# Kernel tuning notes

Measured on AMD Instinct MI355X. Metric: run time of the kernel, lower is better.

Reference implementation:

```python
import jax, jax.numpy as jnp
import numpy as np

B, T, V, D, H = 128, 512, 32000, 300, 128


def setup_inputs() -> dict:
    key = jax.random.key(0)
    ks = jax.random.split(key, 10)
    s = 0.05
    return {
        "encoder_input": jax.random.randint(ks[0], (B, T), 0, V, dtype=jnp.int32),
        "state_fwd": jax.random.normal(ks[1], (B, H), jnp.float32) * s,
        "state_back": jax.random.normal(ks[2], (B, H), jnp.float32) * s,
        "emb": jax.random.normal(ks[3], (V, D), jnp.float32) * s,
        "W_f": jax.random.normal(ks[4], (D, 3 * H), jnp.float32) * s,
        "U_f": jax.random.normal(ks[5], (H, 3 * H), jnp.float32) * s,
        "b_f": jax.random.normal(ks[6], (2, 3 * H), jnp.float32) * s,
        "W_b": jax.random.normal(ks[7], (D, 3 * H), jnp.float32) * s,
        "U_b": jax.random.normal(ks[8], (H, 3 * H), jnp.float32) * s,
        "b_b": jax.random.normal(ks[9], (2, 3 * H), jnp.float32) * s,
    }


def _gru(x, h0, W, U, b):
    # Keras GRU, reset_after=True, eval mode (dropout off).
    b_i, b_r = b[0], b[1]
    xp = jnp.einsum('btd,dg->btg', x, W) + b_i      # precompute input projections [B,T,3H]
    xp = jnp.swapaxes(xp, 0, 1)                     # time-major [T,B,3H]

    def step(h, xpt):
        rec = h @ U + b_r                           # [B,3H]
        xz, xr, xh = jnp.split(xpt, 3, axis=-1)
        rz, rr, rh = jnp.split(rec, 3, axis=-1)
        z = jax.nn.sigmoid(xz + rz)
        r = jax.nn.sigmoid(xr + rr)
        hh = jnp.tanh(xh + r * rh)
        hn = z * h + (1.0 - z) * hh
        return hn, hn

    hT, ys = jax.lax.scan(step, h0, xp)
    return jnp.swapaxes(ys, 0, 1), hT               # [B,T,H], [B,H]


def reference(encoder_input, state_fwd, state_back, emb, W_f, U_f, b_f, W_b, U_b, b_b):
    x = emb[encoder_input]                          # [B,T,D] embedding lookup
    out_f, h_f = _gru(x, state_fwd, W_f, U_f, b_f)
    out_b_rev, h_b = _gru(x[:, ::-1], state_back, W_b, U_b, b_b)
    out_b = out_b_rev[:, ::-1]
    encoder_output = jnp.concatenate([out_f, out_b], axis=-1)  # [B,T,2H]
    return encoder_output, h_f, h_b
```

## Files before the change

### kernel.cpp

```cpp
#include <hip/hip_runtime.h>
#include <stddef.h>

#define BB   128
#define TT   512
#define VV   32000
#define DD   300
#define HH   128
#define G3   384
#define NC   768

typedef __fp16 half_t;
typedef __fp16 half2_t __attribute__((ext_vector_type(2)));
typedef _Float16 f16x8 __attribute__((ext_vector_type(8)));
typedef float    f32x4 __attribute__((ext_vector_type(4)));

union FragF {
    f16x8    v;
    _Float16 h[8];
    f32x4    f4;
};

#define ASTR 40
__global__ __launch_bounds__(256) void proj_kernel(
    const float* __restrict__ emb,
    const float* __restrict__ Wf, const float* __restrict__ Wb,
    const float* __restrict__ bf, const float* __restrict__ bb,
    float* __restrict__ P)
{
    __shared__ __align__(16) _Float16 As[128][ASTR];
    __shared__ __align__(16) _Float16 Bs[128][ASTR];

    const int m0 = blockIdx.x * 128;
    const int n0 = blockIdx.y * 128;

    const float* Wsrc;
    const float* bsrc;
    int cb;
    if (n0 < G3) { Wsrc = Wf; bsrc = bf; cb = n0; }
    else         { Wsrc = Wb; bsrc = bb; cb = n0 - G3; }

    const int t  = threadIdx.x;
    const int w  = t >> 6;
    const int l  = t & 63;
    const int lr = l & 15;
    const int lg = l >> 4;

    f32x4 acc[2][8];
    #pragma unroll
    for (int i = 0; i < 2; ++i)
        #pragma unroll
        for (int j = 0; j < 8; ++j)
            acc[i][j] = (f32x4){0.f, 0.f, 0.f, 0.f};

    const int sm = t & 127;
    const int sh = t >> 7;

    for (int kt = 0; kt < 10; ++kt) {
        const int kb = kt * 32 + sh * 16;

        {
            float v[16];
            if (kt < 9) {
                const float4* src = (const float4*)(emb + (size_t)(m0 + sm) * DD + kb);
                float4 v0 = src[0], v1 = src[1], v2 = src[2], v3 = src[3];
                v[0]=v0.x; v[1]=v0.y; v[2]=v0.z; v[3]=v0.w;
                v[4]=v1.x; v[5]=v1.y; v[6]=v1.z; v[7]=v1.w;
                v[8]=v2.x; v[9]=v2.y; v[10]=v2.z; v[11]=v2.w;
                v[12]=v3.x; v[13]=v3.y; v[14]=v3.z; v[15]=v3.w;
            } else {
                #pragma unroll
                for (int j = 0; j < 16; ++j) {
                    int k = kb + j;
                    v[j] = (k < DD) ? emb[(size_t)(m0 + sm) * DD + k] : 0.f;
                }
            }
            half2_t p[8];
            #pragma unroll
            for (int j = 0; j < 8; ++j)
                p[j] = __builtin_amdgcn_cvt_pkrtz(v[2*j], v[2*j+1]);
            *(float4*)&As[sm][sh * 16]     = *(float4*)&p[0];
            *(float4*)&As[sm][sh * 16 + 8] = *(float4*)&p[4];
        }
        {
            float v[16];
            #pragma unroll
            for (int j = 0; j < 16; ++j) {
                int k = kb + j;
                v[j] = (k < DD) ? Wsrc[(size_t)k * G3 + cb + sm] : 0.f;
            }
            half2_t p[8];
            #pragma unroll
            for (int j = 0; j < 8; ++j)
                p[j] = __builtin_amdgcn_cvt_pkrtz(v[2*j], v[2*j+1]);
            *(float4*)&Bs[sm][sh * 16]     = *(float4*)&p[0];
            *(float4*)&Bs[sm][sh * 16 + 8] = *(float4*)&p[4];
        }
        __syncthreads();

        FragF a[2], bfr[8];
        #pragma unroll
        for (int mf = 0; mf < 2; ++mf)
            a[mf].f4 = *(const f32x4*)&As[lr + 16 * (2 * w + mf)][lg * 8];
        #pragma unroll
        for (int nf = 0; nf < 8; ++nf)
            bfr[nf].f4 = *(const f32x4*)&Bs[lr + 16 * nf][lg * 8];
        #pragma unroll
        for (int mf = 0; mf < 2; ++mf)
            #pragma unroll
            for (int nf = 0; nf < 8; ++nf)
                acc[mf][nf] = __builtin_amdgcn_mfma_f32_16x16x32_f16(
                    a[mf].v, bfr[nf].v, acc[mf][nf], 0, 0, 0);
        __syncthreads();
    }

    float bias_v[8];
    #pragma unroll
    for (int nf = 0; nf < 8; ++nf) bias_v[nf] = bsrc[cb + 16 * nf + lr];

    #pragma unroll
    for (int mf = 0; mf < 2; ++mf)
        #pragma unroll
        for (int nf = 0; nf < 8; ++nf)
            #pragma unroll
            for (int r = 0; r < 4; ++r) {
                int row = m0 + 16 * (2 * w + mf) + lg * 4 + r;
                int col = n0 + 16 * nf + lr;
                P[(size_t)row * NC + col] = acc[mf][nf][r] + bias_v[nf];
            }
}

template<int CTRL>
__device__ __forceinline__ float qp_add(float x) {
    union { float f; int i; } a, r;
    a.f = x;
    r.i = __builtin_amdgcn_update_dpp(0, a.i, CTRL, 0xF, 0xF, true);
    return x + r.f;
}

#define BAR() asm volatile("s_waitcnt lgkmcnt(0)\n\ts_barrier" ::: "memory")

__global__ __launch_bounds__(512)
__attribute__((amdgpu_waves_per_eu(2, 2)))
void scan_kernel(
    const int*   __restrict__ tokens,
    const float* __restrict__ state_f, const float* __restrict__ state_b,
    const float* __restrict__ Uf, const float* __restrict__ Ub,
    const float* __restrict__ bf, const float* __restrict__ bb,
    const float* __restrict__ P,
    float* __restrict__ out)
{
    const int b = blockIdx.x;
    const int d = blockIdx.y;
    const int t = threadIdx.x;
    const int s = t & 3;
    const int q = t >> 2;

    const float* U  = d ? Ub : Uf;
    const float* bv = d ? bb : bf;
    const float* st = d ? state_b : state_f;
    const int    cb = d ? G3 : 0;

    __shared__ __align__(16) half_t hs[2][HH];
    __shared__ int tok_s[TT];

    tok_s[t] = tokens[b * TT + t];

    half2_t uz2[16], ur2[16], uh2[16];
    #pragma unroll
    for (int k2 = 0; k2 < 16; ++k2) {
        const float* U0 = U + (size_t)(s * 32 + 2 * k2) * G3;
        const float* U1 = U0 + G3;
        uz2[k2] = __builtin_amdgcn_cvt_pkrtz(U0[q],          U1[q]);
        ur2[k2] = __builtin_amdgcn_cvt_pkrtz(U0[HH + q],     U1[HH + q]);
        uh2[k2] = __builtin_amdgcn_cvt_pkrtz(U0[2 * HH + q], U1[2 * HH + q]);
    }
    const float bz = bv[G3 + q];
    const float br = bv[G3 + HH + q];
    const float bh = bv[G3 + 2 * HH + q];

    float hreg = st[b * HH + q];
    if (t < HH) hs[0][t] = (half_t)st[b * HH + t];
    __syncthreads();

    float xz_n, xr_n, xh_n;
    {
        int tok = tok_s[d ? (TT - 1) : 0];
        const float* pr = P + (size_t)tok * NC + cb;
        xz_n = pr[q]; xr_n = pr[HH + q]; xh_n = pr[2 * HH + q];
    }

    int cur = 0;
    for (int i = 0; i < TT; ++i) {
        const int tcur = d ? (TT - 1 - i) : i;
        const float xz = xz_n, xr = xr_n, xh = xh_n;
        {
            int in1 = (i + 1 < TT) ? (i + 1) : i;
            int tok = tok_s[d ? (TT - 1 - in1) : in1];
            const float* pr = P + (size_t)tok * NC + cb;
            xz_n = pr[q]; xr_n = pr[HH + q]; xh_n = pr[2 * HH + q];
        }

        half2_t hv[16];
        {
            const float4* hp = (const float4*)&hs[cur][s * 32];
            *(float4*)&hv[0]  = hp[0];
            *(float4*)&hv[4]  = hp[1];
            *(float4*)&hv[8]  = hp[2];
            *(float4*)&hv[12] = hp[3];
        }
        float az = 0.f, ar = 0.f, ah = 0.f;
        #pragma unroll
        for (int k2 = 0; k2 < 16; ++k2) {
            az = __builtin_amdgcn_fdot2(hv[k2], uz2[k2], az, false);
            ar = __builtin_amdgcn_fdot2(hv[k2], ur2[k2], ar, false);
            ah = __builtin_amdgcn_fdot2(hv[k2], uh2[k2], ah, false);
        }
        az = qp_add<0xB1>(az); az = qp_add<0x4E>(az);
        ar = qp_add<0xB1>(ar); ar = qp_add<0x4E>(ar);
        ah = qp_add<0xB1>(ah); ah = qp_add<0x4E>(ah);

        float z = __builtin_amdgcn_rcpf(1.f + __expf(-(az + bz + xz)));
        float r = __builtin_amdgcn_rcpf(1.f + __expf(-(ar + br + xr)));
        float ph = xh + r * (ah + bh);
        ph = fminf(fmaxf(ph, -15.f), 15.f);
        float e  = __expf(-2.f * ph);
        float hh = (1.f - e) * __builtin_amdgcn_rcpf(1.f + e);
        float hn = z * hreg + (1.f - z) * hh;
        hreg = hn;

        const int nxt = cur ^ 1;
        if (s == 0) {
            hs[nxt][q] = (half_t)hn;
            out[((size_t)b * TT + tcur) * 256 + d * HH + q] = hn;
        }
        BAR();
        cur = nxt;
    }

    if (s == 0) {
        out[(size_t)BB * TT * 256 + (size_t)d * BB * HH + b * HH + q] = hreg;
    }
}

extern "C" void kernel_launch(void* const* d_in, const int* in_sizes, int n_in,
                              void* d_out, int out_size, void* d_ws, size_t ws_size,
                              hipStream_t stream)
{
    const int*   tokens  = (const int*)  d_in[0];
    const float* state_f = (const float*)d_in[1];
    const float* state_b = (const float*)d_in[2];
    const float* emb     = (const float*)d_in[3];
    const float* W_f     = (const float*)d_in[4];
    const float* U_f     = (const float*)d_in[5];
    const float* b_f     = (const float*)d_in[6];
    const float* W_b     = (const float*)d_in[7];
    const float* U_b     = (const float*)d_in[8];
    const float* b_b     = (const float*)d_in[9];
    float*       out     = (float*)d_out;

    float* P = (float*)d_ws;

    dim3 gp(VV / 128, NC / 128);
    proj_kernel<<<gp, 256, 0, stream>>>(emb, W_f, W_b, b_f, b_b, P);

    dim3 gs(BB, 2);
    scan_kernel<<<gs, 512, 0, stream>>>(tokens, state_f, state_b,
                                        U_f, U_b, b_f, b_b, P, out);
}
```

Before: 427.6 us.

## Use MFMA for recurrent matvec in scan and double-buffer projection tiles

The scan kernel's recurrent h·U product moves from per-thread fdot2 chains plus DPP quad reductions to 16x16x32 f16 MFMA instructions. U fragments stay in registers, each wave owns 16 output columns, and the h row is broadcast across the A operand, so most MFMA rows are redundant work. The next token index is now fetched two steps ahead, and the waves_per_eu hint is dropped. The projection kernel prefetches the next K tile into registers while MFMAs run on the current shared tile, at the cost of an extra barrier per iteration.

```diff
diff --git a/kernel.cpp b/kernel.cpp
--- a/kernel.cpp
+++ b/kernel.cpp
@@ -9,7 +9,6 @@
 #define G3   384
 #define NC   768
 
-typedef __fp16 half_t;
 typedef __fp16 half2_t __attribute__((ext_vector_type(2)));
 typedef _Float16 f16x8 __attribute__((ext_vector_type(8)));
 typedef float    f32x4 __attribute__((ext_vector_type(4)));
@@ -19,6 +18,8 @@
     _Float16 h[8];
     f32x4    f4;
 };
+
+#define BAR() asm volatile("s_waitcnt lgkmcnt(0)\n\ts_barrier" ::: "memory")
 
 #define ASTR 40
 __global__ __launch_bounds__(256) void proj_kernel(
@@ -55,47 +56,51 @@
     const int sm = t & 127;
     const int sh = t >> 7;
 
+    float va[16], vb[16];
+
+#define LOAD_TILE(KT)                                                         \
+    {                                                                         \
+        const int kb_ = (KT) * 32 + sh * 16;                                  \
+        if ((KT) < 9) {                                                       \
+            const float4* srcA = (const float4*)(emb + (size_t)(m0 + sm) * DD + kb_); \
+            float4 a0 = srcA[0], a1 = srcA[1], a2 = srcA[2], a3 = srcA[3];    \
+            va[0]=a0.x; va[1]=a0.y; va[2]=a0.z; va[3]=a0.w;                   \
+            va[4]=a1.x; va[5]=a1.y; va[6]=a1.z; va[7]=a1.w;                   \
+            va[8]=a2.x; va[9]=a2.y; va[10]=a2.z; va[11]=a2.w;                 \
+            va[12]=a3.x; va[13]=a3.y; va[14]=a3.z; va[15]=a3.w;               \
+            _Pragma("unroll")                                                 \
+            for (int j = 0; j < 16; ++j)                                      \
+                vb[j] = Wsrc[(size_t)(kb_ + j) * G3 + cb + sm];               \
+        } else {                                                              \
+            _Pragma("unroll")                                                 \
+            for (int j = 0; j < 16; ++j) {                                    \
+                int k_ = kb_ + j;                                             \
+                va[j] = (k_ < DD) ? emb[(size_t)(m0 + sm) * DD + k_] : 0.f;   \
+                vb[j] = (k_ < DD) ? Wsrc[(size_t)k_ * G3 + cb + sm] : 0.f;    \
+            }                                                                 \
+        }                                                                     \
+    }
+
+#define STORE_TILE()                                                          \
+    {                                                                         \
+        half2_t pa[8], pb[8];                                                 \
+        _Pragma("unroll")                                                     \
+        for (int j = 0; j < 8; ++j) {                                         \
+            pa[j] = __builtin_amdgcn_cvt_pkrtz(va[2*j], va[2*j+1]);           \
+            pb[j] = __builtin_amdgcn_cvt_pkrtz(vb[2*j], vb[2*j+1]);           \
+        }                                                                     \
+        *(float4*)&As[sm][sh * 16]     = *(float4*)&pa[0];                    \
+        *(float4*)&As[sm][sh * 16 + 8] = *(float4*)&pa[4];                    \
+        *(float4*)&Bs[sm][sh * 16]     = *(float4*)&pb[0];                    \
+        *(float4*)&Bs[sm][sh * 16 + 8] = *(float4*)&pb[4];                    \
+    }
+
+    LOAD_TILE(0);
+    STORE_TILE();
+    BAR();
+
     for (int kt = 0; kt < 10; ++kt) {
-        const int kb = kt * 32 + sh * 16;
-
-        {
-            float v[16];
-            if (kt < 9) {
-                const float4* src = (const float4*)(emb + (size_t)(m0 + sm) * DD + kb);
-                float4 v0 = src[0], v1 = src[1], v2 = src[2], v3 = src[3];
-                v[0]=v0.x; v[1]=v0.y; v[2]=v0.z; v[3]=v0.w;
-                v[4]=v1.x; v[5]=v1.y; v[6]=v1.z; v[7]=v1.w;
-                v[8]=v2.x; v[9]=v2.y; v[10]=v2.z; v[11]=v2.w;
-                v[12]=v3.x; v[13]=v3.y; v[14]=v3.z; v[15]=v3.w;
-            } else {
-                #pragma unroll
-                for (int j = 0; j < 16; ++j) {
-                    int k = kb + j;
-                    v[j] = (k < DD) ? emb[(size_t)(m0 + sm) * DD + k] : 0.f;
-                }
-            }
-            half2_t p[8];
-            #pragma unroll
-            for (int j = 0; j < 8; ++j)
-                p[j] = __builtin_amdgcn_cvt_pkrtz(v[2*j], v[2*j+1]);
-            *(float4*)&As[sm][sh * 16]     = *(float4*)&p[0];
-            *(float4*)&As[sm][sh * 16 + 8] = *(float4*)&p[4];
-        }
-        {
-            float v[16];
-            #pragma unroll
-            for (int j = 0; j < 16; ++j) {
-                int k = kb + j;
-                v[j] = (k < DD) ? Wsrc[(size_t)k * G3 + cb + sm] : 0.f;
-            }
-            half2_t p[8];
-            #pragma unroll
-            for (int j = 0; j < 8; ++j)
-                p[j] = __builtin_amdgcn_cvt_pkrtz(v[2*j], v[2*j+1]);
-            *(float4*)&Bs[sm][sh * 16]     = *(float4*)&p[0];
-            *(float4*)&Bs[sm][sh * 16 + 8] = *(float4*)&p[4];
-        }
-        __syncthreads();
+        if (kt < 9) LOAD_TILE(kt + 1);
 
         FragF a[2], bfr[8];
         #pragma unroll
@@ -110,7 +115,9 @@
             for (int nf = 0; nf < 8; ++nf)
                 acc[mf][nf] = __builtin_amdgcn_mfma_f32_16x16x32_f16(
                     a[mf].v, bfr[nf].v, acc[mf][nf], 0, 0, 0);
-        __syncthreads();
+        BAR();
+        if (kt < 9) STORE_TILE();
+        BAR();
     }
 
     float bias_v[8];
@@ -127,21 +134,11 @@
                 int col = n0 + 16 * nf + lr;
                 P[(size_t)row * NC + col] = acc[mf][nf][r] + bias_v[nf];
             }
+#undef LOAD_TILE
+#undef STORE_TILE
 }
 
-template<int CTRL>
-__device__ __forceinline__ float qp_add(float x) {
-    union { float f; int i; } a, r;
-    a.f = x;
-    r.i = __builtin_amdgcn_update_dpp(0, a.i, CTRL, 0xF, 0xF, true);
-    return x + r.f;
-}
-
-#define BAR() asm volatile("s_waitcnt lgkmcnt(0)\n\ts_barrier" ::: "memory")
-
-__global__ __launch_bounds__(512)
-__attribute__((amdgpu_waves_per_eu(2, 2)))
-void scan_kernel(
+__global__ __launch_bounds__(512) void scan_kernel(
     const int*   __restrict__ tokens,
     const float* __restrict__ state_f, const float* __restrict__ state_b,
     const float* __restrict__ Uf, const float* __restrict__ Ub,
@@ -149,96 +146,96 @@
     const float* __restrict__ P,
     float* __restrict__ out)
 {
-    const int b = blockIdx.x;
-    const int d = blockIdx.y;
-    const int t = threadIdx.x;
-    const int s = t & 3;
-    const int q = t >> 2;
+    const int b  = blockIdx.x;
+    const int d  = blockIdx.y;
+    const int t  = threadIdx.x;
+    const int w  = t >> 6;
+    const int l  = t & 63;
+    const int lr = l & 15;
+    const int lg = l >> 4;
+    const int c  = w * 16 + lr;
 
     const float* U  = d ? Ub : Uf;
     const float* bv = d ? bb : bf;
     const float* st = d ? state_b : state_f;
     const int    cb = d ? G3 : 0;
 
-    __shared__ __align__(16) half_t hs[2][HH];
+    __shared__ __align__(16) _Float16 hs[2][HH];
     __shared__ int tok_s[TT];
 
     tok_s[t] = tokens[b * TT + t];
 
-    half2_t uz2[16], ur2[16], uh2[16];
-    #pragma unroll
-    for (int k2 = 0; k2 < 16; ++k2) {
-        const float* U0 = U + (size_t)(s * 32 + 2 * k2) * G3;
-        const float* U1 = U0 + G3;
-        uz2[k2] = __builtin_amdgcn_cvt_pkrtz(U0[q],          U1[q]);
-        ur2[k2] = __builtin_amdgcn_cvt_pkrtz(U0[HH + q],     U1[HH + q]);
-        uh2[k2] = __builtin_amdgcn_cvt_pkrtz(U0[2 * HH + q], U1[2 * HH + q]);
-    }
-    const float bz = bv[G3 + q];
-    const float br = bv[G3 + HH + q];
-    const float bh = bv[G3 + 2 * HH + q];
-
-    float hreg = st[b * HH + q];
-    if (t < HH) hs[0][t] = (half_t)st[b * HH + t];
+    FragF Bz[4], Br[4], Bh[4];
+    #pragma unroll
+    for (int kt = 0; kt < 4; ++kt)
+        #pragma unroll
+        for (int j = 0; j < 8; ++j) {
+            const float* Urow = U + (size_t)(kt * 32 + lg * 8 + j) * G3 + c;
+            Bz[kt].h[j] = (_Float16)Urow[0];
+            Br[kt].h[j] = (_Float16)Urow[HH];
+            Bh[kt].h[j] = (_Float16)Urow[2 * HH];
+        }
+    const float bz = bv[G3 + c];
+    const float brc = bv[G3 + HH + c];
+    const float bhc = bv[G3 + 2 * HH + c];
+
+    float hreg = st[b * HH + c];
+    if (t < HH) hs[0][t] = (_Float16)st[b * HH + t];
     __syncthreads();
 
     float xz_n, xr_n, xh_n;
+    int   tokB;
     {
-        int tok = tok_s[d ? (TT - 1) : 0];
-        const float* pr = P + (size_t)tok * NC + cb;
-        xz_n = pr[q]; xr_n = pr[HH + q]; xh_n = pr[2 * HH + q];
+        int tok0 = tok_s[d ? (TT - 1) : 0];
+        const float* pr = P + (size_t)tok0 * NC + cb + c;
+        xz_n = pr[0]; xr_n = pr[HH]; xh_n = pr[2 * HH];
+        tokB = tok_s[d ? (TT - 2) : 1];
     }
 
     int cur = 0;
-    for (int i = 0; i < TT; ++i) {
-        const int tcur = d ? (TT - 1 - i) : i;
+    for (int it = 0; it < TT; ++it) {
+        const int tcur = d ? (TT - 1 - it) : it;
         const float xz = xz_n, xr = xr_n, xh = xh_n;
         {
-            int in1 = (i + 1 < TT) ? (i + 1) : i;
-            int tok = tok_s[d ? (TT - 1 - in1) : in1];
-            const float* pr = P + (size_t)tok * NC + cb;
-            xz_n = pr[q]; xr_n = pr[HH + q]; xh_n = pr[2 * HH + q];
-        }
-
-        half2_t hv[16];
-        {
-            const float4* hp = (const float4*)&hs[cur][s * 32];
-            *(float4*)&hv[0]  = hp[0];
-            *(float4*)&hv[4]  = hp[1];
-            *(float4*)&hv[8]  = hp[2];
-            *(float4*)&hv[12] = hp[3];
-        }
-        float az = 0.f, ar = 0.f, ah = 0.f;
-        #pragma unroll
-        for (int k2 = 0; k2 < 16; ++k2) {
-            az = __builtin_amdgcn_fdot2(hv[k2], uz2[k2], az, false);
-            ar = __builtin_amdgcn_fdot2(hv[k2], ur2[k2], ar, false);
-            ah = __builtin_amdgcn_fdot2(hv[k2], uh2[k2], ah, false);
-        }
-        az = qp_add<0xB1>(az); az = qp_add<0x4E>(az);
-        ar = qp_add<0xB1>(ar); ar = qp_add<0x4E>(ar);
-        ah = qp_add<0xB1>(ah); ah = qp_add<0x4E>(ah);
-
-        float z = __builtin_amdgcn_rcpf(1.f + __expf(-(az + bz + xz)));
-        float r = __builtin_amdgcn_rcpf(1.f + __expf(-(ar + br + xr)));
-        float ph = xh + r * (ah + bh);
+            const float* pr = P + (size_t)tokB * NC + cb + c;
+            xz_n = pr[0]; xr_n = pr[HH]; xh_n = pr[2 * HH];
+            int i2 = (it + 2 < TT) ? (it + 2) : (TT - 1);
+            tokB = tok_s[d ? (TT - 1 - i2) : i2];
+        }
+
+        FragF a[4];
+        #pragma unroll
+        for (int kt = 0; kt < 4; ++kt)
+            a[kt].f4 = *(const f32x4*)&hs[cur][kt * 32 + lg * 8];
+
+        f32x4 az = {0.f,0.f,0.f,0.f}, ar = {0.f,0.f,0.f,0.f}, ah = {0.f,0.f,0.f,0.f};
+        #pragma unroll
+        for (int kt = 0; kt < 4; ++kt) {
+            az = __builtin_amdgcn_mfma_f32_16x16x32_f16(a[kt].v, Bz[kt].v, az, 0, 0, 0);
+            ar = __builtin_amdgcn_mfma_f32_16x16x32_f16(a[kt].v, Br[kt].v, ar, 0, 0, 0);
+            ah = __builtin_amdgcn_mfma_f32_16x16x32_f16(a[kt].v, Bh[kt].v, ah, 0, 0, 0);
+        }
+
+        float z  = __builtin_amdgcn_rcpf(1.f + __expf(-(az[0] + bz  + xz)));
+        float r  = __builtin_amdgcn_rcpf(1.f + __expf(-(ar[0] + brc + xr)));
+        float ph = xh + r * (ah[0] + bhc);
         ph = fminf(fmaxf(ph, -15.f), 15.f);
-        float e  = __expf(-2.f * ph);
-        float hh = (1.f - e) * __builtin_amdgcn_rcpf(1.f + e);
-        float hn = z * hreg + (1.f - z) * hh;
+        float e   = __expf(-2.f * ph);
+        float hhv = (1.f - e) * __builtin_amdgcn_rcpf(1.f + e);
+        float hn  = z * hreg + (1.f - z) * hhv;
         hreg = hn;
 
         const int nxt = cur ^ 1;
-        if (s == 0) {
-            hs[nxt][q] = (half_t)hn;
-            out[((size_t)b * TT + tcur) * 256 + d * HH + q] = hn;
+        if (lg == 0) {
+            hs[nxt][c] = (_Float16)hn;
+            out[((size_t)b * TT + tcur) * 256 + d * HH + c] = hn;
         }
         BAR();
         cur = nxt;
     }
 
-    if (s == 0) {
-        out[(size_t)BB * TT * 256 + (size_t)d * BB * HH + b * HH + q] = hreg;
+    if (lg == 0) {
+        out[(size_t)BB * TT * 256 + (size_t)d * BB * HH + b * HH + c] = hreg;
     }
 }
 
```

New measurement: 356.3 us. -16.7%, faster.
